# Kernel optimization log

Measured on AMD Instinct MI355X. Metric: run time of the kernel, lower is better.

The kernel has to match this reference:

```python
import jax, jax.numpy as jnp
import numpy as np

# --- APPM / NMS pipeline constants (3 ratio groups on the 28x28 mixed feature map) ---
RATIOS = [4, 6, 8]            # square sliding-window sizes in feature cells
N_LIST = [2, 3, 2]            # proposals kept per group (proposalN = 7)
IOU_THRESHS = [0.25, 0.25, 0.25]
FM_SIZE = 28                  # mixed feature map spatial size
STRIDE = 16                   # 448 / 28: feature cell -> image pixels
IMG = 448
PROPOSAL_N = sum(N_LIST)
GROUP_SIZES = [(FM_SIZE - r + 1) ** 2 for r in RATIOS]


def make_coordinates():
    """[x0, y0, x1, y1] image-space boxes for every sliding window, all groups concatenated."""
    coords = []
    for r in RATIOS:
        n = FM_SIZE - r + 1
        ii, jj = np.meshgrid(np.arange(n), np.arange(n), indexing='ij')
        x0 = (ii.ravel() * STRIDE).astype(np.int32)
        y0 = (jj.ravel() * STRIDE).astype(np.int32)
        coords.append(np.stack([x0, y0, x0 + r * STRIDE, y0 + r * STRIDE], axis=1))
    return np.concatenate(coords, axis=0).astype(np.int32)   # (1595, 4)


def window_scores_from_fm(fm):
    """AvgPool2d(r, stride=1) then sum over channels == reduce_window over channel-summed map."""
    s = jnp.sum(fm, axis=1)  # (B, H, W)
    outs = []
    for r in RATIOS:
        w = jax.lax.reduce_window(s, 0.0, jax.lax.add, (1, r, r), (1, 1, 1), 'VALID') / float(r * r)
        outs.append(w.reshape(s.shape[0], -1))
    return jnp.concatenate(outs, axis=1)  # (B, sum(GROUP_SIZES))


def nms_group(scores, boxes, n_sel, thresh):
    """Greedy IoU NMS, exactly the inclusive (+1) box math of the source nms()."""
    areas = (boxes[:, 2] - boxes[:, 0] + 1.0) * (boxes[:, 3] - boxes[:, 1] + 1.0)

    def body(k, carry):
        sc, idxs = carry
        i = jnp.argmax(sc)                       # highest remaining score
        idxs = idxs.at[k].set(i.astype(jnp.int32))
        b = boxes[i]
        xx0 = jnp.maximum(boxes[:, 0], b[0]); yy0 = jnp.maximum(boxes[:, 1], b[1])
        xx1 = jnp.minimum(boxes[:, 2], b[2]); yy1 = jnp.minimum(boxes[:, 3], b[3])
        w = xx1 - xx0 + 1.0; h = yy1 - yy0 + 1.0
        inter = jnp.where((w < 0) | (h < 0), 0.0, w * h)
        iou = inter / (areas + areas[i] - inter)
        sc = jnp.where(iou > thresh, -jnp.inf, sc)  # suppress (selected box has iou=1 -> removed)
        return sc, idxs

    _, idxs = jax.lax.fori_loop(0, n_sel, body, (scores, jnp.zeros((n_sel,), jnp.int32)))
    return idxs


def select_proposals(all_scores, coordinates):
    parts = []
    off = 0
    for ng, n_sel, th in zip(GROUP_SIZES, N_LIST, IOU_THRESHS):
        sc = all_scores[:, off:off + ng]
        bx = coordinates[off:off + ng].astype(jnp.float32)
        idx = jax.vmap(lambda s: nms_group(s, bx, n_sel, th))(sc) + off
        parts.append(idx)
        off += ng
    return jnp.concatenate(parts, axis=1)  # (B, PROPOSAL_N) global window indices


def crop_windows(x, coordinates, indices):
    """Gather-crop each proposal window from the raw image, bilinear-resize to 448x448."""
    outs = []
    col = 0
    for r, n_sel in zip(RATIOS, N_LIST):
        w = r * STRIDE  # fixed crop size for this ratio group
        idx_g = indices[:, col:col + n_sel]

        def crop_one(img, gi):
            c = coordinates[gi]
            patch = jax.lax.dynamic_slice(img, (0, c[0], c[1]), (3, w, w))
            return jax.image.resize(patch, (3, IMG, IMG), 'bilinear')

        crops = jax.vmap(lambda img, gis: jax.vmap(lambda gi: crop_one(img, gi))(gis))(x, idx_g)
        outs.append(crops)
        col += n_sel
    return jnp.concatenate(outs, axis=1)  # (B, PROPOSAL_N, 3, 448, 448)


def setup_inputs() -> dict:
    key = jax.random.key(0)
    k1, k2, k3, k4 = jax.random.split(key, 4)
    B = 8
    return {
        'x': jax.random.normal(k1, (B, 3, IMG, IMG), jnp.float32),
        'fm': jax.random.normal(k2, (B, 384, FM_SIZE, FM_SIZE), jnp.float32),
        'embedding': jax.random.normal(k3, (B, 2048), jnp.float32),
        'W_cls': jax.random.normal(k4, (2048, 200), jnp.float32) * 0.02,
        'b_cls': jnp.zeros((200,), jnp.float32),
        'coordinates': jnp.asarray(make_coordinates()),
    }


def reference(x, fm, embedding, W_cls, b_cls, coordinates):
    all_scores = window_scores_from_fm(fm)                              # window_scores (B, 1595)
    proposalN_indices = select_proposals(all_scores, coordinates)       # (B, 7) int32
    proposalN_windows_scores = jnp.take_along_axis(all_scores, proposalN_indices, axis=1)
    window_imgs = crop_windows(x, coordinates, proposalN_indices)
    window_imgs = window_imgs.reshape(-1, 3, IMG, IMG)                  # (B*7, 3, 448, 448)
    raw_logits = embedding @ W_cls + b_cls                              # rawcls_net
    return (proposalN_indices, proposalN_windows_scores, all_scores, window_imgs, raw_logits)
```

## Files before the change

### kernel.cpp

```cpp
#include <hip/hip_runtime.h>
#include <math.h>

#define THREADS 256
#define CROP_GRID 944
#define NTASK (56 * 3 * 28)

typedef float f32x4 __attribute__((ext_vector_type(4)));

__global__ __launch_bounds__(THREADS) void fused1_kernel(const float* __restrict__ fm,
                                                         float4* __restrict__ part,
                                                         int cpc, int K,
                                                         const float* __restrict__ emb,
                                                         const float* __restrict__ W,
                                                         float* __restrict__ lpart) {
    int blk = blockIdx.x;
    int t = threadIdx.x;
    if (blk < 8 * K) {
        int b = blk / K, k = blk - b * K;
        if (t >= 196) return;
        const float4* f = (const float4*)(fm + ((size_t)b * 384 + (size_t)k * cpc) * 784);
        float4 acc = {0.0f, 0.0f, 0.0f, 0.0f};
        for (int c = 0; c < cpc; ++c) {
            float4 v = f[(size_t)c * 196 + t];
            acc.x += v.x; acc.y += v.y; acc.z += v.z; acc.w += v.w;
        }
        part[((size_t)b * K + k) * 196 + t] = acc;
    } else {
        int idx = blk - 8 * K;
        int b = idx >> 4, kc = idx & 15;
        if (t >= 200) return;
        const float* e  = emb + (size_t)b * 2048 + kc * 128;
        const float* wp = W + (size_t)kc * 128 * 200 + t;
        float acc = 0.0f;
        #pragma unroll 4
        for (int k = 0; k < 128; ++k)
            acc += e[k] * wp[(size_t)k * 200];
        lpart[((size_t)b * 16 + kc) * 200 + t] = acc;
    }
}

__global__ __launch_bounds__(THREADS) void fused2_kernel(const float4* __restrict__ part,
                                                         int K,
                                                         float* __restrict__ all_scores,
                                                         float* __restrict__ out_idx_f,
                                                         float* __restrict__ out_sc,
                                                         int* __restrict__ ws_idx,
                                                         int* __restrict__ soff,
                                                         const int* __restrict__ coords,
                                                         const float* __restrict__ lpart,
                                                         const float* __restrict__ bias,
                                                         float* __restrict__ logits) {
    __shared__ float4 s4[196];
    __shared__ float  pref[28][29];
    __shared__ float  scl[625];
    __shared__ float  rv[4];
    __shared__ int    ri[4];
    int t = threadIdx.x;

    if (blockIdx.x >= 24) {
        int b = blockIdx.x - 24;
        if (t >= 200) return;
        float acc = bias[t];
        #pragma unroll
        for (int kc = 0; kc < 16; ++kc)
            acc += lpart[((size_t)b * 16 + kc) * 200 + t];
        logits[b * 200 + t] = acc;
        return;
    }

    int b = blockIdx.x / 3, g = blockIdx.x - b * 3;

    if (t < 196) {
        float4 acc = {0.0f, 0.0f, 0.0f, 0.0f};
        #pragma unroll 8
        for (int k = 0; k < K; ++k) {
            float4 v = part[((size_t)b * K + k) * 196 + t];
            acc.x += v.x; acc.y += v.y; acc.z += v.z; acc.w += v.w;
        }
        s4[t] = acc;
    }
    __syncthreads();
    if (t < 28) {
        float4 row[7];
        #pragma unroll
        for (int i = 0; i < 7; ++i) row[i] = s4[t * 7 + i];
        float run = 0.0f;
        pref[t][0] = 0.0f;
        #pragma unroll
        for (int j = 0; j < 28; ++j) {
            run += ((float*)row)[j];
            pref[t][j + 1] = run;
        }
    }
    __syncthreads();

    const int gnA[3]   = {625, 529, 441};
    const int sideA[3] = {25, 23, 21};
    const int rA[3]    = {4, 6, 8};
    const int nselA[3] = {2, 3, 2};
    const int colA[3]  = {0, 2, 5};
    const int goffA[3] = {0, 625, 1154};

    int n = gnA[g], side = sideA[g], r = rA[g];
    int nsel = nselA[g], goff = goffA[g], colbase = colA[g];
    float inv = 1.0f / (float)(r * r);

    for (int loc = t; loc < n; loc += THREADS) {
        int i = loc / side, j = loc % side;
        float acc = 0.0f;
        for (int a = 0; a < r; ++a)
            acc += pref[i + a][j + r] - pref[i + a][j];
        float sv = acc * inv;
        scl[loc] = sv;
        all_scores[b * 1595 + goff + loc] = sv;
    }
    __syncthreads();

    float ext = (float)(r * 16 + 1);
    float A   = ext * ext;
    float rs  = (float)(r * 16);

    for (int k = 0; k < nsel; ++k) {
        float bv = -INFINITY; int bi = 0x7fffffff;
        for (int i = t; i < n; i += THREADS) {
            float v = scl[i];
            if (v > bv || (v == bv && i < bi)) { bv = v; bi = i; }
        }
        #pragma unroll
        for (int m = 1; m < 64; m <<= 1) {
            float ov = __shfl_xor(bv, m, 64);
            int   oi = __shfl_xor(bi, m, 64);
            if (ov > bv || (ov == bv && oi < bi)) { bv = ov; bi = oi; }
        }
        int wv = t >> 6;
        if ((t & 63) == 0) { rv[wv] = bv; ri[wv] = bi; }
        __syncthreads();
        if (t == 0) {
            for (int q = 1; q < 4; ++q) {
                float ov = rv[q]; int oi = ri[q];
                if (ov > bv || (ov == bv && oi < bi)) { bv = ov; bi = oi; }
            }
            ri[0] = bi;
            int outp = b * 7 + colbase + k;
            int gi   = goff + bi;
            out_idx_f[outp] = (float)gi;
            out_sc[outp]    = bv;
            ws_idx[outp]    = gi;
            soff[outp]      = coords[gi * 4 + 0] * 448 + coords[gi * 4 + 1];
        }
        __syncthreads();
        int sel = ri[0];
        int si = sel / side, sj = sel % side;
        float sx0 = si * 16.0f, sy0 = sj * 16.0f;
        float sx1 = sx0 + rs,   sy1 = sy0 + rs;
        for (int i = t; i < n; i += THREADS) {
            int ii = i / side, jj = i % side;
            float x0 = ii * 16.0f, y0 = jj * 16.0f;
            float x1 = x0 + rs,    y1 = y0 + rs;
            float xx0 = fmaxf(x0, sx0), yy0 = fmaxf(y0, sy0);
            float xx1 = fminf(x1, sx1), yy1 = fminf(y1, sy1);
            float w = xx1 - xx0 + 1.0f, h = yy1 - yy0 + 1.0f;
            float inter = (w < 0.0f || h < 0.0f) ? 0.0f : w * h;
            float iou = inter / (A + A - inter);
            if (iou > 0.25f) scl[i] = -INFINITY;
        }
        __syncthreads();
    }
}

__global__ __launch_bounds__(448) void crop_kernel(const float* __restrict__ x,
                                                   const int* __restrict__ soff,
                                                   float* __restrict__ out) {
    __shared__ float lds[2][924];
    int t = threadIdx.x;

    int rr0 = t / 132, xx0 = t - rr0 * 132;
    int i1  = t + 448;
    int rr1 = i1 / 132, xx1 = i1 - rr1 * 132;
    int xx2 = t + 104;
    int row_sub = t / 56;
    int seg     = t - row_sub * 56;
    int ox0 = seg * 8;

    int task = blockIdx.x;
    int cw; float cscale, cwm1; int cS, crlo; float* coutb;
    float rA, rB, rC = 0.0f;
    {
        int p = task / 84, rem = task - p * 84;
        int ch = rem / 28, stripe = rem - ch * 28;
        int b = p / 7, col = p - b * 7;
        int g = (col < 2) ? 0 : ((col < 5) ? 1 : 2);
        cw = (g == 0) ? 64 : ((g == 1) ? 96 : 128);
        cscale = (float)cw * (1.0f / 448.0f);
        cwm1 = (float)(cw - 1);
        cS = stripe * 16;
        float syb = fminf(fmaxf(((float)cS + 0.5f) * cscale - 0.5f, 0.0f), cwm1);
        crlo = (int)syb;
        const float* cbase = x + ((size_t)(b * 3 + ch)) * 200704 + soff[p];
        coutb = out + ((size_t)(p * 3 + ch)) * 200704;
        rA = cbase[(size_t)min(crlo + rr0, cw - 1) * 448 + min(xx0, cw - 1)];
        rB = cbase[(size_t)min(crlo + rr1, cw - 1) * 448 + min(xx1, cw - 1)];
        if (t < 28)
            rC = cbase[(size_t)min(crlo + 6, cw - 1) * 448 + min(xx2, cw - 1)];
    }

    int buf = 0;
    while (true) {
        int nxt = task + CROP_GRID;
        bool has = nxt < NTASK;

        int nw = 0, nrlo = 0, nS = 0, nso = 0, nb3 = 0, np3 = 0;
        float nscale = 0.0f, nwm1 = 0.0f;
        if (has) {
            int p = nxt / 84, rem = nxt - p * 84;
            int ch = rem / 28, stripe = rem - ch * 28;
            int b = p / 7, col = p - b * 7;
            int g = (col < 2) ? 0 : ((col < 5) ? 1 : 2);
            nw = (g == 0) ? 64 : ((g == 1) ? 96 : 128);
            nscale = (float)nw * (1.0f / 448.0f);
            nwm1 = (float)(nw - 1);
            nS = stripe * 16;
            float syb = fminf(fmaxf(((float)nS + 0.5f) * nscale - 0.5f, 0.0f), nwm1);
            nrlo = (int)syb;
            nso = soff[p];
            nb3 = b * 3 + ch;
            np3 = p * 3 + ch;
        }

        lds[buf][t]       = rA;
        lds[buf][t + 448] = rB;
        if (t < 28) lds[buf][t + 896] = rC;
        asm volatile("s_waitcnt lgkmcnt(0)" ::: "memory");
        __builtin_amdgcn_s_barrier();

        float* noutb = nullptr;
        if (has) {
            const float* nbase = x + (size_t)nb3 * 200704 + nso;
            noutb = out + (size_t)np3 * 200704;
            rA = nbase[(size_t)min(nrlo + rr0, nw - 1) * 448 + min(xx0, nw - 1)];
            rB = nbase[(size_t)min(nrlo + rr1, nw - 1) * 448 + min(xx1, nw - 1)];
            if (t < 28)
                rC = nbase[(size_t)min(nrlo + 6, nw - 1) * 448 + min(xx2, nw - 1)];
        }

        {
            float sxb = ((float)ox0 + 0.5f) * cscale - 0.5f;
            float sxc = fminf(fmaxf(sxb, 0.0f), cwm1);
            int   i0  = (int)sxc;
            float txk[8];
            bool  e1[8], e2[8];
            #pragma unroll
            for (int k = 0; k < 8; ++k) {
                float sx = fminf(fmaxf(sxb + (float)k * cscale, 0.0f), cwm1);
                int xi = (int)sx;
                txk[k] = sx - (float)xi;
                int d  = xi - i0;
                e1[k] = (d >= 1);
                e2[k] = (d >= 2);
            }
            const float* lbase = &lds[buf][0];
            #pragma unroll
            for (int half = 0; half < 2; ++half) {
                int oy = cS + half * 8 + row_sub;
                float sy = fminf(fmaxf(((float)oy + 0.5f) * cscale - 0.5f, 0.0f), cwm1);
                int   y0 = (int)sy;
                int   y1 = min(y0 + 1, cw - 1);
                float ty = sy - (float)y0;
                const float* l0 = lbase + (y0 - crlo) * 132 + i0;
                const float* l1 = lbase + (y1 - crlo) * 132 + i0;
                float a0 = l0[0], a1 = l0[1], a2 = l0[2], a3 = l0[3];
                float b0 = l1[0], b1 = l1[1], b2 = l1[2], b3 = l1[3];
                float da0 = a1 - a0, da1 = a2 - a1, da2 = a3 - a2;
                float db0 = b1 - b0, db1 = b2 - b1, db2 = b3 - b2;

                f32x4 res0, res1;
                #pragma unroll
                for (int k = 0; k < 8; ++k) {
                    float av  = e2[k] ? a2  : (e1[k] ? a1  : a0);
                    float dav = e2[k] ? da2 : (e1[k] ? da1 : da0);
                    float bv  = e2[k] ? b2  : (e1[k] ? b1  : b0);
                    float dbv = e2[k] ? db2 : (e1[k] ? db1 : db0);
                    float top = fmaf(txk[k], dav, av);
                    float bot = fmaf(txk[k], dbv, bv);
                    float rr  = top + ty * (bot - top);
                    if (k < 4) res0[k] = rr; else res1[k - 4] = rr;
                }
                float* orow = coutb + (size_t)oy * 448 + ox0;
                *(f32x4*)orow       = res0;
                *(f32x4*)(orow + 4) = res1;
            }
        }

        if (!has) break;
        cw = nw; cscale = nscale; cwm1 = nwm1; cS = nS; crlo = nrlo; coutb = noutb;
        task = nxt;
        buf ^= 1;
    }
}

extern "C" void kernel_launch(void* const* d_in, const int* in_sizes, int n_in,
                              void* d_out, int out_size, void* d_ws, size_t ws_size,
                              hipStream_t stream) {
    const float* x      = (const float*)d_in[0];
    const float* fm     = (const float*)d_in[1];
    const float* emb    = (const float*)d_in[2];
    const float* Wc     = (const float*)d_in[3];
    const float* bc     = (const float*)d_in[4];
    const int*   coords = (const int*)d_in[5];

    float* out        = (float*)d_out;
    float* out_idx    = out;
    float* out_sc     = out + 56;
    float* all_scores = out + 112;
    float* imgs       = out + 12872;
    float* logits     = out + 33731144;

    int K = 32;
    while (K > 1 && ws_size < 1024 + (size_t)8 * K * 784 * 4 + 25600 * 4) K >>= 1;
    int cpc = 384 / K;

    int*    ws_idx = (int*)d_ws;
    int*    soff   = (int*)((char*)d_ws + 256);
    float4* part   = (float4*)((char*)d_ws + 1024);
    float*  lpart  = (float*)((char*)d_ws + 1024 + (size_t)8 * K * 784 * 4);

    fused1_kernel<<<8 * K + 128, THREADS, 0, stream>>>(fm, part, cpc, K, emb, Wc, lpart);
    fused2_kernel<<<32, THREADS, 0, stream>>>(part, K, all_scores, out_idx, out_sc, ws_idx,
                                              soff, coords, lpart, bc, logits);
    crop_kernel<<<CROP_GRID, 448, 0, stream>>>(x, soff, imgs);
}
```

Baseline: 54.25 us.

## Double crop stripe height and split logits GEMV across more K-chunks

The crop kernel now handles 32-row output stripes per task instead of 16. Each task stages a larger source tile in LDS and does four half-iterations, which halves the task count and the per-task overhead. The grid is reduced to 784 blocks. The classifier GEMV is split into up to 64 K-chunks of 32 rows with two accumulators, giving more parallel blocks, and the reduction loop adapts to the chunk count. The risks are a larger LDS footprint lowering occupancy and fewer crop blocks than before.

```diff
diff --git a/kernel.cpp b/kernel.cpp
--- a/kernel.cpp
+++ b/kernel.cpp
@@ -2,8 +2,8 @@
 #include <math.h>
 
 #define THREADS 256
-#define CROP_GRID 944
-#define NTASK (56 * 3 * 28)
+#define CROP_GRID 784
+#define NTASK (56 * 3 * 14)
 
 typedef float f32x4 __attribute__((ext_vector_type(4)));
 
@@ -12,7 +12,8 @@
                                                          int cpc, int K,
                                                          const float* __restrict__ emb,
                                                          const float* __restrict__ W,
-                                                         float* __restrict__ lpart) {
+                                                         float* __restrict__ lpart,
+                                                         int lrows, int LK) {
     int blk = blockIdx.x;
     int t = threadIdx.x;
     if (blk < 8 * K) {
@@ -27,15 +28,19 @@
         part[((size_t)b * K + k) * 196 + t] = acc;
     } else {
         int idx = blk - 8 * K;
-        int b = idx >> 4, kc = idx & 15;
+        int b = idx / LK, kc = idx - b * LK;
         if (t >= 200) return;
-        const float* e  = emb + (size_t)b * 2048 + kc * 128;
-        const float* wp = W + (size_t)kc * 128 * 200 + t;
-        float acc = 0.0f;
-        #pragma unroll 4
-        for (int k = 0; k < 128; ++k)
-            acc += e[k] * wp[(size_t)k * 200];
-        lpart[((size_t)b * 16 + kc) * 200 + t] = acc;
+        const float* e  = emb + (size_t)b * 2048 + kc * lrows;
+        const float* wp = W + (size_t)kc * lrows * 200 + t;
+        float a0 = 0.0f, a1 = 0.0f;
+        #pragma unroll 16
+        for (int k = 0; k < 64; k += 2) {
+            if (k < lrows) {
+                a0 += e[k] * wp[(size_t)k * 200];
+                a1 += e[k + 1] * wp[(size_t)(k + 1) * 200];
+            }
+        }
+        lpart[((size_t)b * LK + kc) * 200 + t] = a0 + a1;
     }
 }
 
@@ -49,7 +54,8 @@
                                                          const int* __restrict__ coords,
                                                          const float* __restrict__ lpart,
                                                          const float* __restrict__ bias,
-                                                         float* __restrict__ logits) {
+                                                         float* __restrict__ logits,
+                                                         int LK) {
     __shared__ float4 s4[196];
     __shared__ float  pref[28][29];
     __shared__ float  scl[625];
@@ -61,9 +67,9 @@
         int b = blockIdx.x - 24;
         if (t >= 200) return;
         float acc = bias[t];
-        #pragma unroll
-        for (int kc = 0; kc < 16; ++kc)
-            acc += lpart[((size_t)b * 16 + kc) * 200 + t];
+        #pragma unroll 16
+        for (int kc = 0; kc < 64; ++kc)
+            if (kc < LK) acc += lpart[((size_t)b * LK + kc) * 200 + t];
         logits[b * 200 + t] = acc;
         return;
     }
@@ -72,7 +78,7 @@
 
     if (t < 196) {
         float4 acc = {0.0f, 0.0f, 0.0f, 0.0f};
-        #pragma unroll 8
+        #pragma unroll 16
         for (int k = 0; k < K; ++k) {
             float4 v = part[((size_t)b * K + k) * 196 + t];
             acc.x += v.x; acc.y += v.y; acc.z += v.z; acc.w += v.w;
@@ -171,37 +177,38 @@
 __global__ __launch_bounds__(448) void crop_kernel(const float* __restrict__ x,
                                                    const int* __restrict__ soff,
                                                    float* __restrict__ out) {
-    __shared__ float lds[2][924];
+    __shared__ float lds[2][1452];
     int t = threadIdx.x;
 
     int rr0 = t / 132, xx0 = t - rr0 * 132;
-    int i1  = t + 448;
-    int rr1 = i1 / 132, xx1 = i1 - rr1 * 132;
-    int xx2 = t + 104;
+    int i1 = t + 448,  rr1 = i1 / 132, xx1 = i1 - rr1 * 132;
+    int i2 = t + 896,  rr2 = i2 / 132, xx2 = i2 - rr2 * 132;
+    int i3 = t + 1344, rr3 = i3 / 132, xx3 = i3 - rr3 * 132;
     int row_sub = t / 56;
     int seg     = t - row_sub * 56;
     int ox0 = seg * 8;
 
     int task = blockIdx.x;
     int cw; float cscale, cwm1; int cS, crlo; float* coutb;
-    float rA, rB, rC = 0.0f;
+    float rA, rB, rC, rD = 0.0f;
     {
-        int p = task / 84, rem = task - p * 84;
-        int ch = rem / 28, stripe = rem - ch * 28;
+        int p = task / 42, rem = task - p * 42;
+        int ch = rem / 14, stripe = rem - ch * 14;
         int b = p / 7, col = p - b * 7;
         int g = (col < 2) ? 0 : ((col < 5) ? 1 : 2);
         cw = (g == 0) ? 64 : ((g == 1) ? 96 : 128);
         cscale = (float)cw * (1.0f / 448.0f);
         cwm1 = (float)(cw - 1);
-        cS = stripe * 16;
+        cS = stripe * 32;
         float syb = fminf(fmaxf(((float)cS + 0.5f) * cscale - 0.5f, 0.0f), cwm1);
         crlo = (int)syb;
         const float* cbase = x + ((size_t)(b * 3 + ch)) * 200704 + soff[p];
         coutb = out + ((size_t)(p * 3 + ch)) * 200704;
         rA = cbase[(size_t)min(crlo + rr0, cw - 1) * 448 + min(xx0, cw - 1)];
         rB = cbase[(size_t)min(crlo + rr1, cw - 1) * 448 + min(xx1, cw - 1)];
-        if (t < 28)
-            rC = cbase[(size_t)min(crlo + 6, cw - 1) * 448 + min(xx2, cw - 1)];
+        rC = cbase[(size_t)min(crlo + rr2, cw - 1) * 448 + min(xx2, cw - 1)];
+        if (t < 108)
+            rD = cbase[(size_t)min(crlo + rr3, cw - 1) * 448 + min(xx3, cw - 1)];
     }
 
     int buf = 0;
@@ -212,14 +219,14 @@
         int nw = 0, nrlo = 0, nS = 0, nso = 0, nb3 = 0, np3 = 0;
         float nscale = 0.0f, nwm1 = 0.0f;
         if (has) {
-            int p = nxt / 84, rem = nxt - p * 84;
-            int ch = rem / 28, stripe = rem - ch * 28;
+            int p = nxt / 42, rem = nxt - p * 42;
+            int ch = rem / 14, stripe = rem - ch * 14;
             int b = p / 7, col = p - b * 7;
             int g = (col < 2) ? 0 : ((col < 5) ? 1 : 2);
             nw = (g == 0) ? 64 : ((g == 1) ? 96 : 128);
             nscale = (float)nw * (1.0f / 448.0f);
             nwm1 = (float)(nw - 1);
-            nS = stripe * 16;
+            nS = stripe * 32;
             float syb = fminf(fmaxf(((float)nS + 0.5f) * nscale - 0.5f, 0.0f), nwm1);
             nrlo = (int)syb;
             nso = soff[p];
@@ -227,9 +234,10 @@
             np3 = p * 3 + ch;
         }
 
-        lds[buf][t]       = rA;
-        lds[buf][t + 448] = rB;
-        if (t < 28) lds[buf][t + 896] = rC;
+        lds[buf][t]        = rA;
+        lds[buf][t + 448]  = rB;
+        lds[buf][t + 896]  = rC;
+        if (t < 108) lds[buf][t + 1344] = rD;
         asm volatile("s_waitcnt lgkmcnt(0)" ::: "memory");
         __builtin_amdgcn_s_barrier();
 
@@ -239,8 +247,9 @@
             noutb = out + (size_t)np3 * 200704;
             rA = nbase[(size_t)min(nrlo + rr0, nw - 1) * 448 + min(xx0, nw - 1)];
             rB = nbase[(size_t)min(nrlo + rr1, nw - 1) * 448 + min(xx1, nw - 1)];
-            if (t < 28)
-                rC = nbase[(size_t)min(nrlo + 6, nw - 1) * 448 + min(xx2, nw - 1)];
+            rC = nbase[(size_t)min(nrlo + rr2, nw - 1) * 448 + min(xx2, nw - 1)];
+            if (t < 108)
+                rD = nbase[(size_t)min(nrlo + rr3, nw - 1) * 448 + min(xx3, nw - 1)];
         }
 
         {
@@ -260,7 +269,7 @@
             }
             const float* lbase = &lds[buf][0];
             #pragma unroll
-            for (int half = 0; half < 2; ++half) {
+            for (int half = 0; half < 4; ++half) {
                 int oy = cS + half * 8 + row_sub;
                 float sy = fminf(fmaxf(((float)oy + 0.5f) * cscale - 0.5f, 0.0f), cwm1);
                 int   y0 = (int)sy;
@@ -316,16 +325,22 @@
     float* logits     = out + 33731144;
 
     int K = 32;
-    while (K > 1 && ws_size < 1024 + (size_t)8 * K * 784 * 4 + 25600 * 4) K >>= 1;
+    int LK = 64;
+    while (LK > 16 && ws_size < 1024 + (size_t)8 * K * 784 * 4 + (size_t)8 * LK * 200 * 4)
+        LK >>= 1;
+    while (K > 1 && ws_size < 1024 + (size_t)8 * K * 784 * 4 + (size_t)8 * LK * 200 * 4)
+        K >>= 1;
     int cpc = 384 / K;
+    int lrows = 2048 / LK;
 
     int*    ws_idx = (int*)d_ws;
     int*    soff   = (int*)((char*)d_ws + 256);
     float4* part   = (float4*)((char*)d_ws + 1024);
     float*  lpart  = (float*)((char*)d_ws + 1024 + (size_t)8 * K * 784 * 4);
 
-    fused1_kernel<<<8 * K + 128, THREADS, 0, stream>>>(fm, part, cpc, K, emb, Wc, lpart);
+    fused1_kernel<<<8 * K + 8 * LK, THREADS, 0, stream>>>(fm, part, cpc, K, emb, Wc,
+                                                          lpart, lrows, LK);
     fused2_kernel<<<32, THREADS, 0, stream>>>(part, K, all_scores, out_idx, out_sc, ws_idx,
-                                              soff, coords, lpart, bc, logits);
+                                              soff, coords, lpart, bc, logits, LK);
     crop_kernel<<<CROP_GRID, 448, 0, stream>>>(x, soff, imgs);
 }
```

Measured after the change: 58.30 us. 1.07x slower.
